# Performance work log

Hardware: AMD Instinct MI355X
Metric: run time of the kernel (lower is better)

## Reference

```python
import jax, jax.numpy as jnp
import numpy as np

EPS = 1e-6
BN_EPS = 1e-5
STAGES = 10


def setup_inputs() -> dict:
    key = jax.random.key(0)
    ks = jax.random.split(key, 8)
    B, L, C, K, INNER = 16, 2048, 256, 64, 4096
    x = jax.random.normal(ks[0], (B, L, C), jnp.float32)
    group_tokens = jax.random.normal(ks[1], (B, K, C), jnp.float32)
    mu0 = jax.random.normal(ks[2], (1, K, C), jnp.float32) * np.sqrt(2.0 / C)
    mu0 = mu0 / (EPS + jnp.linalg.norm(mu0, axis=2, keepdims=True))
    w1 = jax.random.normal(ks[3], (INNER, C), jnp.float32) * 0.02
    b1 = jnp.zeros((INNER,), jnp.float32)
    gamma = jnp.ones((INNER,), jnp.float32)
    beta = jnp.zeros((INNER,), jnp.float32)
    bn_mean = jnp.zeros((INNER,), jnp.float32)
    bn_var = jnp.ones((INNER,), jnp.float32)
    w2 = jax.random.normal(ks[4], (C, INNER), jnp.float32) * 0.02
    b2 = jnp.zeros((C,), jnp.float32)
    return {"x": x, "group_tokens": group_tokens, "mu0": mu0, "w1": w1,
            "b1": b1, "gamma": gamma, "beta": beta, "bn_mean": bn_mean,
            "bn_var": bn_var, "w2": w2, "b2": b2}


def _em_loop(x, mu):
    # x: [B,L,C], mu: [B,K,C]; 10-step soft-clustering fixed point (no_grad in torch)
    def step(carry, _):
        mu, _ = carry
        z = jax.nn.softmax(jnp.einsum('blc,bkc->blk', x, mu), axis=-1)  # [B,L,K]
        z = z / (EPS + z.sum(axis=1, keepdims=True))
        mu = jnp.einsum('blk,blc->bkc', z, x)
        mu = mu / (EPS + jnp.linalg.norm(mu, axis=2, keepdims=True))
        return (mu, z), None
    z0 = jnp.zeros(x.shape[:2] + (mu.shape[1],), x.dtype)
    (mu, z), _ = jax.lax.scan(step, (mu, z0), None, length=STAGES)
    return jax.lax.stop_gradient(mu), jax.lax.stop_gradient(z)


def _project_mlp(x, w1, b1, gamma, beta, bn_mean, bn_var, w2, b2):
    # Conv1d(k=1) == channelwise linear; BN in eval mode with running stats
    h = jnp.einsum('blc,ic->bli', x, w1) + b1                 # [B,L,INNER]
    h = (h - bn_mean) * (gamma / jnp.sqrt(bn_var + BN_EPS)) + beta
    h = jax.nn.relu(h)
    return jnp.einsum('bli,oi->blo', h, w2) + b2              # [B,L,C]


def reference(x, group_tokens, mu0, w1, b1, gamma, beta, bn_mean, bn_var, w2, b2):
    B = group_tokens.shape[0]
    mu = jnp.broadcast_to(mu0, (B,) + mu0.shape[1:])
    mu, z = _em_loop(x, mu)
    recon_x = jnp.einsum('blk,bkc->blc', z, mu)
    recon_x = _project_mlp(recon_x, w1, b1, gamma, beta, bn_mean, bn_var, w2, b2)
    new_z = jax.nn.softmax(jnp.einsum('blc,bkc->blk', x, mu), axis=-1)
    attn_map = new_z / (EPS + new_z.sum(axis=1, keepdims=True))  # [B,L,K]
    attn_map = jnp.transpose(attn_map, (0, 2, 1))[:, None]       # [B,1,K,L]
    return mu, attn_map, recon_x
```

## Files before the change

### kernel.cpp

```cpp
#include <hip/hip_runtime.h>

constexpr int B_ = 16, L_ = 2048, C_ = 256, K_ = 64, INNER_ = 4096;
constexpr int NCH = 32;
constexpr int RPB = 64;
#define EPSF 1e-6f

typedef __attribute__((ext_vector_type(8)))  short bf16x8;
typedef __attribute__((ext_vector_type(4)))  float f32x4;
typedef __attribute__((ext_vector_type(16))) float f32x16;
typedef _Float16 f16;
typedef __attribute__((ext_vector_type(8))) _Float16 f16x8;
typedef __attribute__((ext_vector_type(4))) _Float16 f16x4;

__device__ __forceinline__ unsigned short f2bf(float f) {
  union { float f; unsigned u; } v; v.f = f;
  unsigned r = v.u + 0x7fffu + ((v.u >> 16) & 1u);
  return (unsigned short)(r >> 16);
}

__device__ __forceinline__ void gload16(const void* src, void* lds) {
  __builtin_amdgcn_global_load_lds(
      (const __attribute__((address_space(1))) unsigned*)src,
      (__attribute__((address_space(3))) unsigned*)lds, 16, 0, 0);
}

__global__ __launch_bounds__(256) void k_pre(
    const float* __restrict__ w1, const float* __restrict__ w2,
    const float* __restrict__ gamma, const float* __restrict__ beta,
    const float* __restrict__ bmean, const float* __restrict__ bvar,
    const float* __restrict__ b1, const float* __restrict__ mu0,
    unsigned short* __restrict__ w1fr, unsigned short* __restrict__ w2fr,
    f16* __restrict__ bnshH, f16* __restrict__ muF)
{
  int i = blockIdx.x * 256 + threadIdx.x;
  if (i < INNER_ * C_) {
    int j = i & 7, l31 = (i >> 3) & 31;
    {
      int l5 = (i >> 8) & 1, ks = (i >> 9) & 15, ih = (i >> 13) & 1, ic = i >> 14;
      int r1 = ic * 64 + ih * 32 + l31;
      int c1 = ks * 16 + 4 * l5 + 8 * (j >> 2) + (j & 3);
      float sc = gamma[r1] * rsqrtf(bvar[r1] + 1e-5f);
      w1fr[i] = f2bf(w1[(size_t)r1 * C_ + c1] * sc);
    }
    {
      int ot = (i >> 8) & 7, l5 = (i >> 11) & 1, g = i >> 12;
      int o = ot * 32 + l31;
      int ii = g * 16 + 4 * l5 + 8 * (j >> 2) + (j & 3);
      w2fr[i] = f2bf(w2[(size_t)o * INNER_ + ii]);
    }
  }
  if (i < B_ * K_ * C_) muF[i] = (f16)mu0[i & (K_ * C_ - 1)];
  if (i < INNER_) {
    float sc = gamma[i] * rsqrtf(bvar[i] + 1e-5f);
    bnshH[i] = (f16)fmaf(b1[i] - bmean[i], sc, beta[i]);
  }
}

__global__ __launch_bounds__(256) void k_xT(const float* __restrict__ x,
                                            f16* __restrict__ xf, f16* __restrict__ xTf)
{
  __shared__ float ts[64][65];
  int l0 = blockIdx.x * 64, c0 = blockIdx.y * 64, b = blockIdx.z;
  int t = threadIdx.x;
  for (int p = 0; p < 16; ++p) {
    int e = t + p * 256, i = e >> 6, j = e & 63;
    float vv = x[((size_t)b * L_ + l0 + i) * C_ + c0 + j];
    ts[i][j] = vv;
    xf[((size_t)b * L_ + l0 + i) * C_ + c0 + j] = (f16)vv;
  }
  __syncthreads();
  for (int p = 0; p < 16; ++p) {
    int e = t + p * 256, i = e >> 6, j = e & 63;
    xTf[((size_t)b * C_ + c0 + i) * L_ + l0 + j] = (f16)ts[j][i];
  }
}

template<bool DO_MU, bool WRITE_Z>
__global__ __launch_bounds__(256, 2) void k_em(
    const f16* __restrict__ xf, const f16* __restrict__ xTf,
    const f16* __restrict__ muF, f16* __restrict__ zout,
    float* __restrict__ cp, f16* __restrict__ part)
{
  __shared__ f16 mu_s[K_ * C_];
  __shared__ f16 zT_s[K_ * RPB];
  __shared__ f16 xtile[C_ * RPB];
  __shared__ float cpart[4][K_];

  int t = threadIdx.x, b = blockIdx.y, chn = blockIdx.x, l0 = chn * RPB;
  int w = t >> 6, lane = t & 63, l15 = lane & 15, g = lane >> 4;

#pragma unroll
  for (int q = 0; q < 8; ++q) {
    int s = q * 256 + t, k = s >> 5, sl = s & 31;
    gload16(muF + (size_t)b * (K_ * C_) + k * C_ + ((sl ^ (k & 15)) << 3), mu_s + s * 8);
  }
  __builtin_amdgcn_sched_barrier(0);
  f16x8 xfr[8];
  const f16* xr = xf + ((size_t)b * L_ + l0 + w * 16 + l15) * C_ + g * 8;
#pragma unroll
  for (int ck = 0; ck < 8; ++ck) xfr[ck] = *(const f16x8*)(xr + ck * 32);
  __builtin_amdgcn_sched_barrier(0);
  if (DO_MU) {
#pragma unroll
    for (int q = 0; q < 8; ++q) {
      int s = q * 256 + t, c = s >> 3, sl = s & 7;
      gload16(xTf + (size_t)(b * C_ + c) * L_ + l0 + ((sl ^ (c & 7)) << 3), xtile + s * 8);
    }
    __builtin_amdgcn_sched_barrier(0);
    asm volatile("s_waitcnt vmcnt(8)" ::: "memory");
  } else {
    asm volatile("s_waitcnt vmcnt(0)" ::: "memory");
  }
  __builtin_amdgcn_s_barrier();
  __builtin_amdgcn_sched_barrier(0);

  f32x4 acc[4];
#pragma unroll
  for (int mt = 0; mt < 4; ++mt)
#pragma unroll
    for (int j = 0; j < 4; ++j) acc[mt][j] = 0.f;
#pragma unroll
  for (int ck = 0; ck < 8; ++ck) {
#pragma unroll
    for (int mt = 0; mt < 4; ++mt) {
      f16x8 a = *(const f16x8*)(mu_s + (mt * 16 + l15) * C_ + (((ck * 4 + g) ^ l15) << 3));
      acc[mt] = __builtin_amdgcn_mfma_f32_16x16x32_f16(a, xfr[ck], acc[mt], 0, 0, 0);
    }
  }

  float z[4][4];
  {
    float mx = acc[0][0];
#pragma unroll
    for (int mt = 0; mt < 4; ++mt)
#pragma unroll
      for (int jj = 0; jj < 4; ++jj) mx = fmaxf(mx, acc[mt][jj]);
    mx = fmaxf(mx, __shfl_xor(mx, 16, 64));
    mx = fmaxf(mx, __shfl_xor(mx, 32, 64));
    float sm = 0.f;
#pragma unroll
    for (int mt = 0; mt < 4; ++mt)
#pragma unroll
      for (int jj = 0; jj < 4; ++jj) {
        float e = __expf(acc[mt][jj] - mx);
        z[mt][jj] = e; sm += e;
      }
    sm += __shfl_xor(sm, 16, 64);
    sm += __shfl_xor(sm, 32, 64);
    float inv = 1.f / sm;
#pragma unroll
    for (int mt = 0; mt < 4; ++mt)
#pragma unroll
      for (int jj = 0; jj < 4; ++jj) z[mt][jj] *= inv;
  }

#pragma unroll
  for (int mt = 0; mt < 4; ++mt)
#pragma unroll
    for (int jj = 0; jj < 4; ++jj) {
      float v = z[mt][jj];
      v += __shfl_xor(v, 1, 64); v += __shfl_xor(v, 2, 64);
      v += __shfl_xor(v, 4, 64); v += __shfl_xor(v, 8, 64);
      if (l15 == 0) cpart[w][mt * 16 + g * 4 + jj] = v;
    }

#pragma unroll
  for (int mt = 0; mt < 4; ++mt)
#pragma unroll
    for (int jj = 0; jj < 4; ++jj) {
      int k = mt * 16 + g * 4 + jj;
      int tl = w * 16 + l15;
      f16 h = (f16)z[mt][jj];
      if (DO_MU)   zT_s[k * RPB + (((tl >> 3) ^ (k & 7)) << 3) + (tl & 7)] = h;
      if (WRITE_Z) zout[((size_t)b * L_ + l0 + tl) * K_ + k] = h;
    }
  __syncthreads();

  if (t < K_) {
    float s = 0.f;
#pragma unroll
    for (int q = 0; q < 4; ++q) s += cpart[q][t];
    cp[(size_t)chn * (B_ * K_) + b * K_ + t] = s;
  }

  if (DO_MU) {
    f32x4 a3[4][4];
#pragma unroll
    for (int mt = 0; mt < 4; ++mt)
#pragma unroll
      for (int nt = 0; nt < 4; ++nt)
#pragma unroll
        for (int j = 0; j < 4; ++j) a3[mt][nt][j] = 0.f;
    int cb = w * 64;
#pragma unroll
    for (int ks = 0; ks < 2; ++ks) {
      f16x8 az[4], bx[4];
#pragma unroll
      for (int mt = 0; mt < 4; ++mt)
        az[mt] = *(const f16x8*)(zT_s + (mt * 16 + l15) * RPB + (((ks * 4 + g) ^ (l15 & 7)) << 3));
#pragma unroll
      for (int nt = 0; nt < 4; ++nt) {
        int c = cb + nt * 16 + l15;
        bx[nt] = *(const f16x8*)(xtile + c * RPB + (((ks * 4 + g) ^ (c & 7)) << 3));
      }
#pragma unroll
      for (int mt = 0; mt < 4; ++mt)
#pragma unroll
        for (int nt = 0; nt < 4; ++nt)
          a3[mt][nt] = __builtin_amdgcn_mfma_f32_16x16x32_f16(az[mt], bx[nt], a3[mt][nt], 0, 0, 0);
    }
    f16* pp = part + (((size_t)chn * B_ + b) * K_) * C_;
#pragma unroll
    for (int mt = 0; mt < 4; ++mt)
#pragma unroll
      for (int nt = 0; nt < 4; ++nt)
#pragma unroll
        for (int jj = 0; jj < 4; ++jj)
          pp[(size_t)(mt * 16 + g * 4 + jj) * C_ + cb + nt * 16 + l15] = (f16)a3[mt][nt][jj];
  }
}

template<bool LAST>
__global__ __launch_bounds__(256) void k_mufin(
    const f16* __restrict__ part, const float* __restrict__ cp,
    f16* __restrict__ muF, f16* __restrict__ muT,
    float* __restrict__ zsA, float* __restrict__ outmu)
{
  int b = blockIdx.x >> 4, kg = blockIdx.x & 15, t = threadIdx.x;
  int kr = t >> 6, c4 = t & 63, k = kg * 4 + kr;
  float a0 = 0.f, a1 = 0.f, a2 = 0.f, a3 = 0.f;
#pragma unroll
  for (int chn = 0; chn < NCH; ++chn) {
    f16x4 p = *(const f16x4*)(part + (((size_t)chn * B_ + b) * K_ + k) * C_ + c4 * 4);
    a0 += (float)p[0]; a1 += (float)p[1]; a2 += (float)p[2]; a3 += (float)p[3];
  }
  float zs = 0.f;
#pragma unroll
  for (int chn = 0; chn < NCH; ++chn) zs += cp[(size_t)chn * (B_ * K_) + b * K_ + k];
  float sc = 1.f / (EPSF + zs);
  a0 *= sc; a1 *= sc; a2 *= sc; a3 *= sc;
  float ssq = a0 * a0 + a1 * a1 + a2 * a2 + a3 * a3;
#pragma unroll
  for (int off = 32; off >= 1; off >>= 1) ssq += __shfl_xor(ssq, off, 64);
  float inv = 1.f / (EPSF + sqrtf(ssq));
  a0 *= inv; a1 *= inv; a2 *= inv; a3 *= inv;
  size_t base = (size_t)(b * K_ + k) * C_ + c4 * 4;
  f16x4 hm; hm[0] = (f16)a0; hm[1] = (f16)a1; hm[2] = (f16)a2; hm[3] = (f16)a3;
  *(f16x4*)(muF + base) = hm;
  if (c4 == 0) zsA[b * K_ + k] = zs;
  if (LAST) {
    *(float4*)(outmu + base) = make_float4(a0, a1, a2, a3);
    muT[((size_t)b * C_ + c4 * 4 + 0) * K_ + k] = hm[0];
    muT[((size_t)b * C_ + c4 * 4 + 1) * K_ + k] = hm[1];
    muT[((size_t)b * C_ + c4 * 4 + 2) * K_ + k] = hm[2];
    muT[((size_t)b * C_ + c4 * 4 + 3) * K_ + k] = hm[3];
  }
}

__global__ __launch_bounds__(256) void k_attn(
    const f16* __restrict__ zB, const float* __restrict__ cpB, float* __restrict__ attn)
{
  __shared__ float zt[64][68];
  __shared__ float inv_s[K_];
  int b = blockIdx.y, l0 = blockIdx.x * 64, t = threadIdx.x;
  if (t < K_) {
    float zs = 0.f;
#pragma unroll
    for (int chn = 0; chn < NCH; ++chn) zs += cpB[(size_t)chn * (B_ * K_) + b * K_ + t];
    inv_s[t] = 1.f / (EPSF + zs);
  }
  for (int p = 0; p < 16; ++p) {
    int e = t + p * 256, lo = e >> 6, k = e & 63;
    zt[lo][k] = (float)zB[((size_t)b * L_ + l0 + lo) * K_ + k];
  }
  __syncthreads();
  int lo = t & 63, kb = t >> 6;
  for (int p = 0; p < 16; ++p) {
    int k = kb * 16 + p;
    attn[((size_t)b * K_ + k) * L_ + l0 + lo] = zt[lo][k] * inv_s[k];
  }
}

constexpr int W1S_OFF  = 0;
constexpr int W2S_OFF  = 65536;
constexpr int BNS_OFF  = 131072;
constexpr int ZINV_OFF = 139264;
constexpr int POOL_SZ  = 139520;

__global__ __launch_bounds__(512, 2) void k_mlp(
    const f16* __restrict__ zA,
    const f16* __restrict__ muT,
    const float* __restrict__ zsA,
    const unsigned short* __restrict__ w1fr,
    const unsigned short* __restrict__ w2fr,
    const f16* __restrict__ bnshH, const float* __restrict__ b2,
    float* __restrict__ outr)
{
  __shared__ __align__(16) char pool[POOL_SZ];
  unsigned short* w1s = (unsigned short*)(pool + W1S_OFF);
  unsigned short* w2s = (unsigned short*)(pool + W2S_OFF);
  f16* bns_s          = (f16*)(pool + BNS_OFF);
  float* zinv_s       = (float*)(pool + ZINV_OFF);
  f16* muT_s          = (f16*)(pool + W1S_OFF + 32768);
  f16* z_s            = (f16*)(pool + W2S_OFF + 32768);

  int t = threadIdx.x, w = t >> 6, lane = t & 63, l31 = lane & 31, l5 = lane >> 5;
  int rb = blockIdx.x * 128, b = rb >> 11, l0 = rb & 2047;
  int tt = w & 3, ih = w >> 2;

#define STAGE(ic, buf)                                                    \
  {                                                                       \
    _Pragma("unroll")                                                     \
    for (int q = 0; q < 4; ++q) {                                         \
      int d2 = q * 512 + t;                                               \
      gload16(w1fr + (size_t)(ic) * 16384 + d2 * 8,                       \
              w1s + (size_t)(buf) * 16384 + d2 * 8);                      \
    }                                                                     \
    _Pragma("unroll")                                                     \
    for (int q = 0; q < 4; ++q) {                                         \
      int d2 = q * 512 + t;                                               \
      gload16(w2fr + (size_t)(ic) * 16384 + d2 * 8,                       \
              w2s + (size_t)(buf) * 16384 + d2 * 8);                      \
    }                                                                     \
  }

  if (t < K_) zinv_s[t] = 1.f / (EPSF + zsA[b * K_ + t]);
  __builtin_amdgcn_sched_barrier(0);
#pragma unroll
  for (int q = 0; q < 4; ++q) {
    int s = q * 512 + t, c = s >> 3, sl = s & 7;
    gload16(muT + ((size_t)b * C_ + c) * K_ + ((sl ^ (c & 7)) << 3), muT_s + s * 8);
  }
#pragma unroll
  for (int q = 0; q < 2; ++q) {
    int s = q * 512 + t, tok = s >> 3, sl = s & 7;
    gload16(zA + ((size_t)b * L_ + l0 + tok) * K_ + ((sl ^ (tok & 7)) << 3), z_s + s * 8);
  }
  gload16(bnshH + t * 8, bns_s + t * 8);
  __builtin_amdgcn_sched_barrier(0);
  STAGE(0, 0);
  __builtin_amdgcn_sched_barrier(0);
  asm volatile("s_waitcnt vmcnt(8) lgkmcnt(0)" ::: "memory");
  __builtin_amdgcn_s_barrier();
  __builtin_amdgcn_sched_barrier(0);

  bf16x8 rc[16];
  {
    f16x8 bz[4];
#pragma unroll
    for (int kk = 0; kk < 4; ++kk) {
      int tok = tt * 32 + l31;
      f16x8 zr = *(const f16x8*)(z_s + tok * 64 + (((kk * 2 + l5) ^ (tok & 7)) << 3));
      f16x8 sc2;
#pragma unroll
      for (int e = 0; e < 8; ++e)
        sc2[e] = (f16)((float)zr[e] * zinv_s[kk * 16 + l5 * 8 + e]);
      bz[kk] = sc2;
    }
    f32x16 d[8];
#pragma unroll
    for (int m = 0; m < 8; ++m)
#pragma unroll
      for (int r = 0; r < 16; ++r) d[m][r] = 0.f;
#pragma unroll
    for (int kk = 0; kk < 4; ++kk) {
#pragma unroll
      for (int m = 0; m < 8; ++m) {
        int c = m * 32 + l31;
        f16x8 am = *(const f16x8*)(muT_s + c * 64 + (((kk * 2 + l5) ^ (c & 7)) << 3));
        d[m] = __builtin_amdgcn_mfma_f32_32x32x16_f16(am, bz[kk], d[m], 0, 0, 0);
      }
    }
    union Uf { unsigned u[4]; bf16x8 v; } rcU[16];
#pragma unroll
    for (int m = 0; m < 8; ++m)
#pragma unroll
      for (int q = 0; q < 8; ++q) {
        unsigned u = (unsigned)f2bf(d[m][2 * q]) | ((unsigned)f2bf(d[m][2 * q + 1]) << 16);
        rcU[2 * m + (q >> 2)].u[q & 3] = u;
      }
#pragma unroll
    for (int ks = 0; ks < 16; ++ks) rc[ks] = rcU[ks].v;
  }
  asm volatile("s_waitcnt lgkmcnt(0)" ::: "memory");
  __builtin_amdgcn_s_barrier();
  __builtin_amdgcn_sched_barrier(0);

  f32x16 acc2[8];
#pragma unroll
  for (int ot = 0; ot < 8; ++ot)
#pragma unroll
    for (int r = 0; r < 16; ++r) acc2[ot][r] = 0.f;

  const unsigned short* p1base = w1s + ih * 8192 + l5 * 256 + l31 * 8;
  const unsigned short* p2base = w2s + ih * 8192 + l5 * 2048 + l31 * 8;

  for (int ic = 0; ic < 64; ++ic) {
    int cur = ic & 1;
    asm volatile("s_waitcnt vmcnt(0)" ::: "memory");
    __builtin_amdgcn_s_barrier();
    __builtin_amdgcn_sched_barrier(0);
    if (ic < 63) STAGE(ic + 1, cur ^ 1);
    __builtin_amdgcn_sched_barrier(0);

    f32x16 h0, h1;
#pragma unroll
    for (int r = 0; r < 16; ++r) { h0[r] = 0.f; h1[r] = 0.f; }
    const unsigned short* p1 = p1base + cur * 16384;
    __builtin_amdgcn_s_setprio(1);
#pragma unroll
    for (int ks = 0; ks < 16; ++ks) {
      bf16x8 a1 = *(const bf16x8*)(p1 + ks * 512);
      if (ks & 1) h1 = __builtin_amdgcn_mfma_f32_32x32x16_bf16(a1, rc[ks], h1, 0, 0, 0);
      else        h0 = __builtin_amdgcn_mfma_f32_32x32x16_bf16(a1, rc[ks], h0, 0, 0, 0);
    }
    __builtin_amdgcn_s_setprio(0);
#pragma unroll
    for (int r = 0; r < 16; ++r) h0[r] += h1[r];

    f16x4 bnv[4];
#pragma unroll
    for (int q = 0; q < 4; ++q)
      bnv[q] = *(const f16x4*)(bns_s + ic * 64 + ih * 32 + 8 * q + 4 * l5);
    unsigned pk[8];
#pragma unroll
    for (int q = 0; q < 4; ++q) {
#pragma unroll
      for (int pr = 0; pr < 2; ++pr) {
        int r0 = q * 4 + pr * 2;
        float v0 = fmaxf(h0[r0]     + (float)bnv[q][pr * 2],     0.f);
        float v1 = fmaxf(h0[r0 + 1] + (float)bnv[q][pr * 2 + 1], 0.f);
        pk[q * 2 + pr] = (unsigned)f2bf(v0) | ((unsigned)f2bf(v1) << 16);
      }
    }
    union Uf { unsigned u[4]; bf16x8 v; };
    Uf bfr0, bfr1;
#pragma unroll
    for (int m = 0; m < 4; ++m) { bfr0.u[m] = pk[m]; bfr1.u[m] = pk[4 + m]; }

    const unsigned short* p2 = p2base + cur * 16384;
    __builtin_amdgcn_s_setprio(1);
#pragma unroll
    for (int s = 0; s < 2; ++s) {
      bf16x8 bfv = s ? bfr1.v : bfr0.v;
#pragma unroll
      for (int ot = 0; ot < 8; ++ot) {
        bf16x8 a2 = *(const bf16x8*)(p2 + s * 4096 + ot * 256);
        acc2[ot] = __builtin_amdgcn_mfma_f32_32x32x16_bf16(a2, bfv, acc2[ot], 0, 0, 0);
      }
    }
    __builtin_amdgcn_s_setprio(0);
  }
#undef STAGE

  __syncthreads();
  float* red = (float*)pool;
  if (ih == 1) {
#pragma unroll
    for (int ot = 0; ot < 8; ++ot)
#pragma unroll
      for (int r = 0; r < 16; ++r)
        red[((tt * 8 + ot) * 16 + r) * 64 + lane] = acc2[ot][r];
  }
  __syncthreads();
  if (ih == 0) {
    int tok = rb + tt * 32 + l31;
#pragma unroll
    for (int ot = 0; ot < 8; ++ot) {
#pragma unroll
      for (int r = 0; r < 16; ++r)
        acc2[ot][r] += red[((tt * 8 + ot) * 16 + r) * 64 + lane];
#pragma unroll
      for (int q = 0; q < 4; ++q) {
        int o = ot * 32 + 8 * q + 4 * l5;
        float4 bias = *(const float4*)(b2 + o);
        f32x4 v;
        v[0] = acc2[ot][q * 4 + 0] + bias.x;
        v[1] = acc2[ot][q * 4 + 1] + bias.y;
        v[2] = acc2[ot][q * 4 + 2] + bias.z;
        v[3] = acc2[ot][q * 4 + 3] + bias.w;
        *(f32x4*)(outr + (size_t)tok * C_ + o) = v;
      }
    }
  }
}

extern "C" void kernel_launch(void* const* d_in, const int* in_sizes, int n_in,
                              void* d_out, int out_size, void* d_ws, size_t ws_size,
                              hipStream_t stream)
{
  const float* x     = (const float*)d_in[0];
  const float* mu0   = (const float*)d_in[2];
  const float* w1    = (const float*)d_in[3];
  const float* b1    = (const float*)d_in[4];
  const float* gamma = (const float*)d_in[5];
  const float* beta  = (const float*)d_in[6];
  const float* bmean = (const float*)d_in[7];
  const float* bvar  = (const float*)d_in[8];
  const float* w2    = (const float*)d_in[9];
  const float* b2    = (const float*)d_in[10];
  float* out = (float*)d_out;

  char* wsb = (char*)d_ws;
  f16* part = (f16*)(wsb + 0);
  f16* zB   = part;
  f16* zA   = (f16*)(wsb + 16777216);
  f16* xf   = (f16*)(wsb + 20971520);
  f16* xTf  = (f16*)(wsb + 37748736);
  unsigned short* w1fr = (unsigned short*)(wsb + 54525952);
  unsigned short* w2fr = (unsigned short*)(wsb + 56623104);
  f16*   muF   = (f16*)(wsb + 58720256);
  f16*   muT   = (f16*)(wsb + 59244544);
  f16*   bnshH = (f16*)(wsb + 59768832);
  float* cpA   = (float*)(wsb + 59777024);
  float* cpB   = (float*)(wsb + 59908096);
  float* zsA   = (float*)(wsb + 60039168);

  k_pre<<<4096, 256, 0, stream>>>(w1, w2, gamma, beta, bmean, bvar, b1, mu0,
                                  w1fr, w2fr, bnshH, muF);
  k_xT<<<dim3(32, 4, 16), 256, 0, stream>>>(x, xf, xTf);

  for (int s = 0; s < 10; ++s) {
    if (s == 9) k_em<true, true ><<<dim3(NCH, 16), 256, 0, stream>>>(xf, xTf, muF, zA, cpA, part);
    else        k_em<true, false><<<dim3(NCH, 16), 256, 0, stream>>>(xf, xTf, muF, zA, cpA, part);
    if (s == 9) k_mufin<true ><<<256, 256, 0, stream>>>(part, cpA, muF, muT, zsA, out);
    else        k_mufin<false><<<256, 256, 0, stream>>>(part, cpA, muF, muT, zsA, out);
  }
  k_em<false, true><<<dim3(NCH, 16), 256, 0, stream>>>(xf, xTf, muF, zB, cpB, part);
  k_attn<<<dim3(32, 16), 256, 0, stream>>>(zB, cpB, out + 262144);
  k_mlp<<<256, 512, 0, stream>>>(zA, muT, zsA, w1fr, w2fr, bnshH, b2, out + 2359296);
}
```

Before: 351.5 us.

## Double EM row chunk to 128 with 512-thread blocks and fuse prep kernels

The EM kernel now processes 128 rows per block with 8 waves instead of 64 rows with 4 waves. That halves the number of chunks and so halves the per-chunk partial mu and cluster-sum buffers written by k_em and reduced by k_mufin on every iteration. The mu-update GEMM is re-tiled so each wave covers 32 channels over 4 k-steps, and the zT swizzle is widened to match. The weight prep and x transpose kernels are merged into one launch to remove a kernel boundary. The cost is fewer, larger blocks: 256 blocks with larger LDS use may leave CUs less occupied and hide latency less well.

```diff
diff --git a/kernel.cpp b/kernel.cpp
--- a/kernel.cpp
+++ b/kernel.cpp
@@ -1,8 +1,8 @@
 #include <hip/hip_runtime.h>
 
 constexpr int B_ = 16, L_ = 2048, C_ = 256, K_ = 64, INNER_ = 4096;
-constexpr int NCH = 32;
-constexpr int RPB = 64;
+constexpr int NCH = 16;
+constexpr int RPB = 128;
 #define EPSF 1e-6f
 
 typedef __attribute__((ext_vector_type(8)))  short bf16x8;
@@ -24,74 +24,78 @@
       (__attribute__((address_space(3))) unsigned*)lds, 16, 0, 0);
 }
 
-__global__ __launch_bounds__(256) void k_pre(
+__global__ __launch_bounds__(256) void k_prext(
+    const float* __restrict__ x,
     const float* __restrict__ w1, const float* __restrict__ w2,
     const float* __restrict__ gamma, const float* __restrict__ beta,
     const float* __restrict__ bmean, const float* __restrict__ bvar,
     const float* __restrict__ b1, const float* __restrict__ mu0,
     unsigned short* __restrict__ w1fr, unsigned short* __restrict__ w2fr,
-    f16* __restrict__ bnshH, f16* __restrict__ muF)
-{
-  int i = blockIdx.x * 256 + threadIdx.x;
-  if (i < INNER_ * C_) {
-    int j = i & 7, l31 = (i >> 3) & 31;
-    {
-      int l5 = (i >> 8) & 1, ks = (i >> 9) & 15, ih = (i >> 13) & 1, ic = i >> 14;
-      int r1 = ic * 64 + ih * 32 + l31;
-      int c1 = ks * 16 + 4 * l5 + 8 * (j >> 2) + (j & 3);
-      float sc = gamma[r1] * rsqrtf(bvar[r1] + 1e-5f);
-      w1fr[i] = f2bf(w1[(size_t)r1 * C_ + c1] * sc);
-    }
-    {
-      int ot = (i >> 8) & 7, l5 = (i >> 11) & 1, g = i >> 12;
-      int o = ot * 32 + l31;
-      int ii = g * 16 + 4 * l5 + 8 * (j >> 2) + (j & 3);
-      w2fr[i] = f2bf(w2[(size_t)o * INNER_ + ii]);
-    }
-  }
-  if (i < B_ * K_ * C_) muF[i] = (f16)mu0[i & (K_ * C_ - 1)];
-  if (i < INNER_) {
-    float sc = gamma[i] * rsqrtf(bvar[i] + 1e-5f);
-    bnshH[i] = (f16)fmaf(b1[i] - bmean[i], sc, beta[i]);
-  }
-}
-
-__global__ __launch_bounds__(256) void k_xT(const float* __restrict__ x,
-                                            f16* __restrict__ xf, f16* __restrict__ xTf)
+    f16* __restrict__ bnshH, f16* __restrict__ muF,
+    f16* __restrict__ xf, f16* __restrict__ xTf)
 {
   __shared__ float ts[64][65];
-  int l0 = blockIdx.x * 64, c0 = blockIdx.y * 64, b = blockIdx.z;
-  int t = threadIdx.x;
-  for (int p = 0; p < 16; ++p) {
-    int e = t + p * 256, i = e >> 6, j = e & 63;
-    float vv = x[((size_t)b * L_ + l0 + i) * C_ + c0 + j];
-    ts[i][j] = vv;
-    xf[((size_t)b * L_ + l0 + i) * C_ + c0 + j] = (f16)vv;
-  }
-  __syncthreads();
-  for (int p = 0; p < 16; ++p) {
-    int e = t + p * 256, i = e >> 6, j = e & 63;
-    xTf[((size_t)b * C_ + c0 + i) * L_ + l0 + j] = (f16)ts[j][i];
+  int bid = blockIdx.x, t = threadIdx.x;
+  if (bid < 4096) {
+    int i = bid * 256 + t;
+    if (i < INNER_ * C_) {
+      int j = i & 7, l31 = (i >> 3) & 31;
+      {
+        int l5 = (i >> 8) & 1, ks = (i >> 9) & 15, ih = (i >> 13) & 1, ic = i >> 14;
+        int r1 = ic * 64 + ih * 32 + l31;
+        int c1 = ks * 16 + 4 * l5 + 8 * (j >> 2) + (j & 3);
+        float sc = gamma[r1] * rsqrtf(bvar[r1] + 1e-5f);
+        w1fr[i] = f2bf(w1[(size_t)r1 * C_ + c1] * sc);
+      }
+      {
+        int ot = (i >> 8) & 7, l5 = (i >> 11) & 1, g = i >> 12;
+        int o = ot * 32 + l31;
+        int ii = g * 16 + 4 * l5 + 8 * (j >> 2) + (j & 3);
+        w2fr[i] = f2bf(w2[(size_t)o * INNER_ + ii]);
+      }
+    }
+    if (i < B_ * K_ * C_) muF[i] = (f16)mu0[i & (K_ * C_ - 1)];
+    if (i < INNER_) {
+      float sc = gamma[i] * rsqrtf(bvar[i] + 1e-5f);
+      bnshH[i] = (f16)fmaf(b1[i] - bmean[i], sc, beta[i]);
+    }
+  } else {
+    int b2 = bid - 4096;
+    int l0 = (b2 & 31) * 64, c0 = ((b2 >> 5) & 3) * 64, b = b2 >> 7;
+    for (int p = 0; p < 16; ++p) {
+      int e = t + p * 256, i = e >> 6, j = e & 63;
+      float vv = x[((size_t)b * L_ + l0 + i) * C_ + c0 + j];
+      ts[i][j] = vv;
+      xf[((size_t)b * L_ + l0 + i) * C_ + c0 + j] = (f16)vv;
+    }
+    __syncthreads();
+    for (int p = 0; p < 16; ++p) {
+      int e = t + p * 256, i = e >> 6, j = e & 63;
+      xTf[((size_t)b * C_ + c0 + i) * L_ + l0 + j] = (f16)ts[j][i];
+    }
   }
 }
 
 template<bool DO_MU, bool WRITE_Z>
-__global__ __launch_bounds__(256, 2) void k_em(
-    const f16* __restrict__ xf, const f16* __restrict__ xTf,
-    const f16* __restrict__ muF, f16* __restrict__ zout,
-    float* __restrict__ cp, f16* __restrict__ part)
+__global__ __launch_bounds__(512, 2) void k_em(
+    const f16* __restrict__ xf,
+    const f16* __restrict__ xTf,
+    const f16* __restrict__ muF,
+    f16* __restrict__ zout,
+    float* __restrict__ cp,
+    f16* __restrict__ part)
 {
   __shared__ f16 mu_s[K_ * C_];
   __shared__ f16 zT_s[K_ * RPB];
   __shared__ f16 xtile[C_ * RPB];
-  __shared__ float cpart[4][K_];
+  __shared__ float cpart[8][K_];
 
   int t = threadIdx.x, b = blockIdx.y, chn = blockIdx.x, l0 = chn * RPB;
   int w = t >> 6, lane = t & 63, l15 = lane & 15, g = lane >> 4;
 
 #pragma unroll
-  for (int q = 0; q < 8; ++q) {
-    int s = q * 256 + t, k = s >> 5, sl = s & 31;
+  for (int q = 0; q < 4; ++q) {
+    int s = q * 512 + t, k = s >> 5, sl = s & 31;
     gload16(muF + (size_t)b * (K_ * C_) + k * C_ + ((sl ^ (k & 15)) << 3), mu_s + s * 8);
   }
   __builtin_amdgcn_sched_barrier(0);
@@ -103,13 +107,13 @@
   if (DO_MU) {
 #pragma unroll
     for (int q = 0; q < 8; ++q) {
-      int s = q * 256 + t, c = s >> 3, sl = s & 7;
+      int s = q * 512 + t, c = s >> 4, sl = s & 15;
       gload16(xTf + (size_t)(b * C_ + c) * L_ + l0 + ((sl ^ (c & 7)) << 3), xtile + s * 8);
     }
     __builtin_amdgcn_sched_barrier(0);
+    asm volatile("s_waitcnt vmcnt(16)" ::: "memory");
+  } else {
     asm volatile("s_waitcnt vmcnt(8)" ::: "memory");
-  } else {
-    asm volatile("s_waitcnt vmcnt(0)" ::: "memory");
   }
   __builtin_amdgcn_s_barrier();
   __builtin_amdgcn_sched_barrier(0);
@@ -171,7 +175,7 @@
       int k = mt * 16 + g * 4 + jj;
       int tl = w * 16 + l15;
       f16 h = (f16)z[mt][jj];
-      if (DO_MU)   zT_s[k * RPB + (((tl >> 3) ^ (k & 7)) << 3) + (tl & 7)] = h;
+      if (DO_MU)   zT_s[k * RPB + (((tl >> 3) ^ (k & 15)) << 3) + (tl & 7)] = h;
       if (WRITE_Z) zout[((size_t)b * L_ + l0 + tl) * K_ + k] = h;
     }
   __syncthreads();
@@ -179,41 +183,41 @@
   if (t < K_) {
     float s = 0.f;
 #pragma unroll
-    for (int q = 0; q < 4; ++q) s += cpart[q][t];
+    for (int q = 0; q < 8; ++q) s += cpart[q][t];
     cp[(size_t)chn * (B_ * K_) + b * K_ + t] = s;
   }
 
   if (DO_MU) {
-    f32x4 a3[4][4];
+    f32x4 a3[4][2];
 #pragma unroll
     for (int mt = 0; mt < 4; ++mt)
 #pragma unroll
-      for (int nt = 0; nt < 4; ++nt)
+      for (int nt = 0; nt < 2; ++nt)
 #pragma unroll
         for (int j = 0; j < 4; ++j) a3[mt][nt][j] = 0.f;
-    int cb = w * 64;
-#pragma unroll
-    for (int ks = 0; ks < 2; ++ks) {
-      f16x8 az[4], bx[4];
+    int cb = w * 32;
+#pragma unroll
+    for (int ks = 0; ks < 4; ++ks) {
+      f16x8 az[4], bx[2];
 #pragma unroll
       for (int mt = 0; mt < 4; ++mt)
-        az[mt] = *(const f16x8*)(zT_s + (mt * 16 + l15) * RPB + (((ks * 4 + g) ^ (l15 & 7)) << 3));
-#pragma unroll
-      for (int nt = 0; nt < 4; ++nt) {
+        az[mt] = *(const f16x8*)(zT_s + (mt * 16 + l15) * RPB + (((ks * 4 + g) ^ l15) << 3));
+#pragma unroll
+      for (int nt = 0; nt < 2; ++nt) {
         int c = cb + nt * 16 + l15;
         bx[nt] = *(const f16x8*)(xtile + c * RPB + (((ks * 4 + g) ^ (c & 7)) << 3));
       }
 #pragma unroll
       for (int mt = 0; mt < 4; ++mt)
 #pragma unroll
-        for (int nt = 0; nt < 4; ++nt)
+        for (int nt = 0; nt < 2; ++nt)
           a3[mt][nt] = __builtin_amdgcn_mfma_f32_16x16x32_f16(az[mt], bx[nt], a3[mt][nt], 0, 0, 0);
     }
     f16* pp = part + (((size_t)chn * B_ + b) * K_) * C_;
 #pragma unroll
     for (int mt = 0; mt < 4; ++mt)
 #pragma unroll
-      for (int nt = 0; nt < 4; ++nt)
+      for (int nt = 0; nt < 2; ++nt)
 #pragma unroll
         for (int jj = 0; jj < 4; ++jj)
           pp[(size_t)(mt * 16 + g * 4 + jj) * C_ + cb + nt * 16 + l15] = (f16)a3[mt][nt][jj];
@@ -504,29 +508,28 @@
   char* wsb = (char*)d_ws;
   f16* part = (f16*)(wsb + 0);
   f16* zB   = part;
-  f16* zA   = (f16*)(wsb + 16777216);
-  f16* xf   = (f16*)(wsb + 20971520);
-  f16* xTf  = (f16*)(wsb + 37748736);
-  unsigned short* w1fr = (unsigned short*)(wsb + 54525952);
-  unsigned short* w2fr = (unsigned short*)(wsb + 56623104);
-  f16*   muF   = (f16*)(wsb + 58720256);
-  f16*   muT   = (f16*)(wsb + 59244544);
-  f16*   bnshH = (f16*)(wsb + 59768832);
-  float* cpA   = (float*)(wsb + 59777024);
-  float* cpB   = (float*)(wsb + 59908096);
-  float* zsA   = (float*)(wsb + 60039168);
-
-  k_pre<<<4096, 256, 0, stream>>>(w1, w2, gamma, beta, bmean, bvar, b1, mu0,
-                                  w1fr, w2fr, bnshH, muF);
-  k_xT<<<dim3(32, 4, 16), 256, 0, stream>>>(x, xf, xTf);
+  f16* zA   = (f16*)(wsb + 8388608);
+  f16* xf   = (f16*)(wsb + 12582912);
+  f16* xTf  = (f16*)(wsb + 29360128);
+  unsigned short* w1fr = (unsigned short*)(wsb + 46137344);
+  unsigned short* w2fr = (unsigned short*)(wsb + 48234496);
+  f16*   muF   = (f16*)(wsb + 50331648);
+  f16*   muT   = (f16*)(wsb + 50855936);
+  f16*   bnshH = (f16*)(wsb + 51380224);
+  float* cpA   = (float*)(wsb + 51388416);
+  float* cpB   = (float*)(wsb + 51453952);
+  float* zsA   = (float*)(wsb + 51519488);
+
+  k_prext<<<6144, 256, 0, stream>>>(x, w1, w2, gamma, beta, bmean, bvar, b1, mu0,
+                                    w1fr, w2fr, bnshH, muF, xf, xTf);
 
   for (int s = 0; s < 10; ++s) {
-    if (s == 9) k_em<true, true ><<<dim3(NCH, 16), 256, 0, stream>>>(xf, xTf, muF, zA, cpA, part);
-    else        k_em<true, false><<<dim3(NCH, 16), 256, 0, stream>>>(xf, xTf, muF, zA, cpA, part);
+    if (s == 9) k_em<true, true ><<<dim3(NCH, 16), 512, 0, stream>>>(xf, xTf, muF, zA, cpA, part);
+    else        k_em<true, false><<<dim3(NCH, 16), 512, 0, stream>>>(xf, xTf, muF, zA, cpA, part);
     if (s == 9) k_mufin<true ><<<256, 256, 0, stream>>>(part, cpA, muF, muT, zsA, out);
     else        k_mufin<false><<<256, 256, 0, stream>>>(part, cpA, muF, muT, zsA, out);
   }
-  k_em<false, true><<<dim3(NCH, 16), 256, 0, stream>>>(xf, xTf, muF, zB, cpB, part);
+  k_em<false, true><<<dim3(NCH, 16), 512, 0, stream>>>(xf, xTf, muF, zB, cpB, part);
   k_attn<<<dim3(32, 16), 256, 0, stream>>>(zB, cpB, out + 262144);
   k_mlp<<<256, 512, 0, stream>>>(zA, muT, zsA, w1fr, w2fr, bnshH, b2, out + 2359296);
 }
```

New measurement: 323.2 us. 1.09x faster.
